# Kernel tuning notes

Measured on AMD Instinct MI355X. Metric: run time of the kernel, lower is better.

The kernel has to match this reference:

```python
import jax, jax.numpy as jnp
import numpy as np

B, S, D_IN, D_OUT = 4, 2048, 1024, 1024

def setup_inputs() -> dict:
    key = jax.random.key(0)
    k0, k1, k2, k3 = jax.random.split(key, 4)
    sc = 1.0 / np.sqrt(D_IN)
    return {
        "x": jax.random.normal(k0, (B, S, D_IN), dtype=jnp.float32),
        "wq": jax.random.normal(k1, (D_OUT, D_IN), dtype=jnp.float32) * sc,
        "wk": jax.random.normal(k2, (D_OUT, D_IN), dtype=jnp.float32) * sc,
        "wv": jax.random.normal(k3, (D_OUT, D_IN), dtype=jnp.float32) * sc,
    }

def reference(x, wq, wk, wv):
    # Linear (no bias): y = x @ W.T, W shaped [d_out, d_in]
    q = jnp.einsum("bsd,ed->bse", x, wq)
    k = jnp.einsum("bsd,ed->bse", x, wk)
    v = jnp.einsum("bsd,ed->bse", x, wv)
    scores = jnp.einsum("bqe,bke->bqk", q, k)  # [B,S,S]
    n = x.shape[1]
    causal = jnp.triu(jnp.ones((n, n), dtype=bool), k=1)  # True above diagonal -> masked
    scores = jnp.where(causal, -jnp.inf, scores)
    attn = jax.nn.softmax(scores / jnp.sqrt(jnp.asarray(k.shape[-1], scores.dtype)), axis=-1)
    # dropout p=0.0 -> identity
    return jnp.einsum("bqk,bke->bqe", attn, v)
```

## Files before the change

kernel.cpp:

```cpp
#include <hip/hip_runtime.h>

#define Bb 4
#define Ss 2048
#define Dd 1024

typedef unsigned short u16;
typedef __bf16 bf16x8 __attribute__((ext_vector_type(8)));
typedef float  f32x4  __attribute__((ext_vector_type(4)));

__device__ inline u16 f2bf(float f) {
  union { float f; unsigned u; } x; x.f = f;
  unsigned u = x.u;
  return (u16)((u + 0x7fffu + ((u >> 16) & 1u)) >> 16);
}
__device__ inline float bf2f(u16 h) {
  union { unsigned u; float f; } x; x.u = ((unsigned)h) << 16;
  return x.f;
}

__device__ static inline void gl_lds16(const u16* g, u16* l) {
  __builtin_amdgcn_global_load_lds((__attribute__((address_space(1))) const void*)g,
                                   (__attribute__((address_space(3))) void*)l,
                                   16, 0, 0);
}

__global__ __launch_bounds__(256) void cast_all(const float* __restrict__ x,
                                                const float* __restrict__ wq,
                                                const float* __restrict__ wk,
                                                const float* __restrict__ wv,
                                                u16* __restrict__ xb,
                                                u16* __restrict__ wb,
                                                float* __restrict__ lsum) {
  int id = blockIdx.x;
  if (id < 8) {
    float4 z = {0.f, 0.f, 0.f, 0.f};
    ((float4*)lsum)[id * 256 + threadIdx.x] = z;
  }
  const float* src; u16* dst; int off;
  if (id < 2048) {
    src = x; dst = xb; off = id * 4096;
  } else {
    int wi = id - 2048;
    int w = wi >> 8;
    src = (w == 0) ? wq : (w == 1) ? wk : wv;
    dst = wb + (size_t)w * Dd * Dd;
    off = (wi & 255) * 4096;
  }
#pragma unroll
  for (int t = 0; t < 4; t++) {
    int i = off + t * 1024 + threadIdx.x * 4;
    float4 v = *(const float4*)(src + i);
    unsigned p0 = (unsigned)f2bf(v.x) | ((unsigned)f2bf(v.y) << 16);
    unsigned p1 = (unsigned)f2bf(v.z) | ((unsigned)f2bf(v.w) << 16);
    uint2 p; p.x = p0; p.y = p1;
    *(uint2*)(dst + i) = p;
  }
}

#define BM 128
#define BN 128

__device__ inline void gemm_tile(const u16* __restrict__ A, int lda,
                                 const u16* __restrict__ Bp, int ldb,
                                 int kBeg, int kEnd,
                                 u16* lds, f32x4 acc[4][4]) {
  u16* lA0 = lds;
  u16* lB0 = lds + 4096;
  u16* lA1 = lds + 8192;
  u16* lB1 = lds + 12288;
  const int tid  = threadIdx.x;
  const int lane = tid & 63, wave = tid >> 6;
  const int quad = lane >> 4, r16 = lane & 15;
  const int wm = (wave & 1) * 64, wn = (wave >> 1) * 64;
  const int r0 = tid >> 2, part = tid & 3;

  for (int k0 = kBeg; k0 < kEnd; k0 += 64) {
    __syncthreads();
#pragma unroll
    for (int q = 0; q < 2; q++) {
      int row = q * 64 + r0;
      int s8 = (q * 256 + tid) * 8;
      const u16* ga = A  + (size_t)row * lda + k0 + part * 8;
      const u16* gb = Bp + (size_t)row * ldb + k0 + part * 8;
      gl_lds16(ga,      lA0 + s8);
      gl_lds16(gb,      lB0 + s8);
      gl_lds16(ga + 32, lA1 + s8);
      gl_lds16(gb + 32, lB1 + s8);
    }
    __syncthreads();
#pragma unroll
    for (int h = 0; h < 2; h++) {
      const u16* la = h ? lA1 : lA0;
      const u16* lb = h ? lB1 : lB0;
      bf16x8 fa[4], fb[4];
#pragma unroll
      for (int t = 0; t < 4; t++)
        fa[t] = *(const bf16x8*)(la + (wm + t * 16 + r16) * 32 + quad * 8);
#pragma unroll
      for (int t = 0; t < 4; t++)
        fb[t] = *(const bf16x8*)(lb + (wn + t * 16 + r16) * 32 + quad * 8);
#pragma unroll
      for (int tm = 0; tm < 4; tm++)
#pragma unroll
        for (int tn = 0; tn < 4; tn++)
          acc[tm][tn] = __builtin_amdgcn_mfma_f32_16x16x32_bf16(fa[tm], fb[tn],
                                                                acc[tm][tn], 0, 0, 0);
    }
  }
}

__global__ __launch_bounds__(256) void qkv_gemm(const u16* __restrict__ xb,
                                                const u16* __restrict__ wb,
                                                u16* __restrict__ qkv) {
  __shared__ __align__(16) u16 shmem[16384];
  const int id  = blockIdx.x;
  const int xcd = id & 7, j = id >> 3;
  const int xt  = j & 7;
  const int yl  = (j >> 3) & 7;
  const int zi  = j >> 6;
  const int y   = xcd * 8 + yl;
  const int row0 = y * BM;
  const int col0 = xt * BN;
  const u16* A  = xb + (size_t)row0 * Dd;
  const u16* Bp = wb + (size_t)zi * Dd * Dd + (size_t)col0 * Dd;
  f32x4 acc[4][4];
  const f32x4 zero = {0.f, 0.f, 0.f, 0.f};
#pragma unroll
  for (int tm = 0; tm < 4; tm++)
#pragma unroll
    for (int tn = 0; tn < 4; tn++) acc[tm][tn] = zero;

  gemm_tile(A, Dd, Bp, Dd, 0, Dd, shmem, acc);

  u16* out = qkv + (size_t)zi * ((size_t)Bb * Ss * Dd);
  const int lane = threadIdx.x & 63, wave = threadIdx.x >> 6;
  const int quad = lane >> 4, r16 = lane & 15;
  const int wm = (wave & 1) * 64, wn = (wave >> 1) * 64;
#pragma unroll
  for (int tm = 0; tm < 4; tm++)
#pragma unroll
    for (int tn = 0; tn < 4; tn++) {
      int rr = row0 + wm + tm * 16 + quad * 4;
      int cc = col0 + wn + tn * 16 + r16;
#pragma unroll
      for (int r = 0; r < 4; r++)
        out[(size_t)(rr + r) * Dd + cc] = f2bf(acc[tm][tn][r]);
    }
}

__global__ __launch_bounds__(256) void scores_fused(const u16* __restrict__ qb,
                                                    const u16* __restrict__ kb,
                                                    const u16* __restrict__ vb,
                                                    u16* __restrict__ sc,
                                                    u16* __restrict__ vt,
                                                    float* __restrict__ lsum) {
  __shared__ __align__(16) u16 shmem[16384];
  const int id = blockIdx.x;
  const int tid = threadIdx.x;

  if (id >= 544) {
    const int bid = id - 544;
    u16 (*t)[72] = (u16(*)[72])shmem;
    for (int u = bid; u < 2048; u += 480) {
      const int b = u >> 9, rem = u & 511;
      const int e0 = (rem >> 5) * 64, s0 = (rem & 31) * 64;
      const u16* src = vb + (size_t)b * Ss * Dd;
      u16* dst = vt + (size_t)b * Dd * Ss;
      if (u != bid) __syncthreads();
#pragma unroll
      for (int gg = tid; gg < 512; gg += 256) {
        int row = gg >> 3, prt = gg & 7;
        uint4 v = *(const uint4*)(src + (size_t)(s0 + row) * Dd + e0 + prt * 8);
        const u16* pv = (const u16*)&v;
#pragma unroll
        for (int jj = 0; jj < 8; jj++) t[prt * 8 + jj][row] = pv[jj];
      }
      __syncthreads();
#pragma unroll
      for (int gg = tid; gg < 512; gg += 256) {
        int ee = gg >> 3, prt = gg & 7;
        uint4 v = *(const uint4*)(&t[ee][prt * 8]);
        *(uint4*)(dst + (size_t)(e0 + ee) * Ss + s0 + prt * 8) = v;
      }
    }
    return;
  }

  const int xcd = id & 7, j = id >> 3;
  const int b = j / 17, tloc = j - b * 17;
  const int t = xcd * 17 + tloc;
  int it = (int)((sqrtf(8.f * (float)t + 1.f) - 1.f) * 0.5f);
  while ((it + 1) * (it + 2) / 2 <= t) it++;
  while (it * (it + 1) / 2 > t) it--;
  const int jt = t - it * (it + 1) / 2;

  const u16* A  = qb + (size_t)b * Ss * Dd + (size_t)it * BM * Dd;
  const u16* Bp = kb + (size_t)b * Ss * Dd + (size_t)jt * BN * Dd;
  f32x4 acc[4][4];
  const f32x4 zero = {0.f, 0.f, 0.f, 0.f};
#pragma unroll
  for (int tm = 0; tm < 4; tm++)
#pragma unroll
    for (int tn = 0; tn < 4; tn++) acc[tm][tn] = zero;

  gemm_tile(A, Dd, Bp, Dd, 0, Dd, shmem, acc);

  u16* out = sc + (size_t)b * Ss * Ss;
  float* lr = lsum + (size_t)b * Ss;
  const int lane = tid & 63, wave = tid >> 6;
  const int quad = lane >> 4, r16 = lane & 15;
  const int wm = (wave & 1) * 64, wn = (wave >> 1) * 64;
#pragma unroll
  for (int tm = 0; tm < 4; tm++) {
    float psum[4] = {0.f, 0.f, 0.f, 0.f};
#pragma unroll
    for (int tn = 0; tn < 4; tn++) {
      int rr = it * BM + wm + tm * 16 + quad * 4;
      int cc = jt * BN + wn + tn * 16 + r16;
#pragma unroll
      for (int r = 0; r < 4; r++) {
        float p = 0.f;
        u16 h = 0;
        if (cc <= rr + r) {
          h = f2bf(__expf(acc[tm][tn][r] * 0.03125f));
          p = bf2f(h);
        }
        out[(size_t)(rr + r) * Ss + cc] = h;
        psum[r] += p;
      }
    }
#pragma unroll
    for (int r = 0; r < 4; r++) {
      float s = psum[r];
      s += __shfl_xor(s, 1);
      s += __shfl_xor(s, 2);
      s += __shfl_xor(s, 4);
      s += __shfl_xor(s, 8);
      if (r16 == 0) {
        int row = it * BM + wm + tm * 16 + quad * 4 + r;
        atomicAdd(&lr[row], s);
      }
    }
  }
}

__global__ __launch_bounds__(256) void pv_gemm(const u16* __restrict__ sc,
                                               const u16* __restrict__ vt,
                                               const float* __restrict__ lsum,
                                               float* __restrict__ out) {
  __shared__ __align__(16) u16 shmem[16384];
  const int idx = blockIdx.x;
  const int xcd = idx & 7, slot = idx >> 3;
  const int qp = slot >> 3, col = slot & 7;
  const int b = qp & 3;
  const int it = (qp >> 2) ? (15 - xcd) : xcd;
  const int row0 = it * BM;
  const int col0 = col * BN;
  const u16* A  = sc + (size_t)b * Ss * Ss + (size_t)row0 * Ss;
  const u16* Bp = vt + (size_t)b * Dd * Ss + (size_t)col0 * Ss;
  f32x4 acc[4][4];
  const f32x4 zero = {0.f, 0.f, 0.f, 0.f};
#pragma unroll
  for (int tm = 0; tm < 4; tm++)
#pragma unroll
    for (int tn = 0; tn < 4; tn++) acc[tm][tn] = zero;

  gemm_tile(A, Ss, Bp, Ss, 0, row0 + BM, shmem, acc);

  float* o = out + (size_t)b * Ss * Dd;
  const float* lr = lsum + (size_t)b * Ss;
  const int lane = threadIdx.x & 63, wave = threadIdx.x >> 6;
  const int quad = lane >> 4, r16 = lane & 15;
  const int wm = (wave & 1) * 64, wn = (wave >> 1) * 64;
#pragma unroll
  for (int tm = 0; tm < 4; tm++) {
    int rbase = row0 + wm + tm * 16 + quad * 4;
    float s0 = 1.f / lr[rbase], s1 = 1.f / lr[rbase + 1];
    float s2 = 1.f / lr[rbase + 2], s3 = 1.f / lr[rbase + 3];
#pragma unroll
    for (int tn = 0; tn < 4; tn++) {
      int cc = col0 + wn + tn * 16 + r16;
      o[(size_t)(rbase + 0) * Dd + cc] = acc[tm][tn][0] * s0;
      o[(size_t)(rbase + 1) * Dd + cc] = acc[tm][tn][1] * s1;
      o[(size_t)(rbase + 2) * Dd + cc] = acc[tm][tn][2] * s2;
      o[(size_t)(rbase + 3) * Dd + cc] = acc[tm][tn][3] * s3;
    }
  }
}

extern "C" void kernel_launch(void* const* d_in, const int* in_sizes, int n_in,
                              void* d_out, int out_size, void* d_ws, size_t ws_size,
                              hipStream_t stream) {
  const float* x  = (const float*)d_in[0];
  const float* wq = (const float*)d_in[1];
  const float* wk = (const float*)d_in[2];
  const float* wv = (const float*)d_in[3];
  float* out = (float*)d_out;
  char* ws = (char*)d_ws;
  if (ws_size < 106987520u) return;

  u16* qkv  = (u16*)(ws);
  u16* sc   = (u16*)(ws + 50331648u);
  u16* xb   = (u16*)(ws + 83886080u);
  u16* vt   = xb;
  u16* wb   = (u16*)(ws + 100663296u);
  float* lsum = (float*)(ws + 106954752u);

  const size_t nQ = (size_t)Bb * Ss * Dd;

  cast_all<<<2816, 256, 0, stream>>>(x, wq, wk, wv, xb, wb, lsum);
  qkv_gemm<<<1536, 256, 0, stream>>>(xb, wb, qkv);
  scores_fused<<<1024, 256, 0, stream>>>(qkv, qkv + nQ, qkv + 2 * nQ, sc, vt, lsum);
  pv_gemm<<<512, 256, 0, stream>>>(sc, vt, lsum, out);
}
```

Before: 233.8 us.

## Replace QKV GEMM with 256x256-tile, 8-wave, 4-stage pipelined kernel

Replaces the 128x128-tile QKV projection GEMM with a 256x256-tile kernel of 512 threads. It uses a 4-deep LDS ring buffer fed by global_load_lds, an XOR-swizzled LDS layout and explicit vmcnt waits, so loads for later K steps overlap the MFMA work. Each half-tile of MFMAs is wrapped in s_setprio, and block ids are remapped so blocks are spread across XCDs. Larger tiles raise operand reuse and cut global traffic, but they use 128KB of LDS and more registers, which limits occupancy and leaves only 384 blocks.

```diff
diff --git a/kernel.cpp b/kernel.cpp
--- a/kernel.cpp
+++ b/kernel.cpp
@@ -22,6 +22,19 @@
   __builtin_amdgcn_global_load_lds((__attribute__((address_space(1))) const void*)g,
                                    (__attribute__((address_space(3))) void*)l,
                                    16, 0, 0);
+}
+
+__device__ static inline void qbar() {
+  asm volatile("" ::: "memory");
+  __builtin_amdgcn_s_barrier();
+  asm volatile("" ::: "memory");
+}
+
+template <int GATEN>
+__device__ __forceinline__ void qk_gate() {
+  if constexpr (GATEN == 8) asm volatile("s_waitcnt vmcnt(8)" ::: "memory");
+  else if constexpr (GATEN == 4) asm volatile("s_waitcnt vmcnt(4)" ::: "memory");
+  else if constexpr (GATEN == 0) asm volatile("s_waitcnt vmcnt(0)" ::: "memory");
 }
 
 __global__ __launch_bounds__(256) void cast_all(const float* __restrict__ x,
@@ -109,43 +122,114 @@
   }
 }
 
-__global__ __launch_bounds__(256) void qkv_gemm(const u16* __restrict__ xb,
-                                                const u16* __restrict__ wb,
-                                                u16* __restrict__ qkv) {
-  __shared__ __align__(16) u16 shmem[16384];
+#define QBK 32
+
+__global__ __launch_bounds__(512, 2) void qkv_gemm256(const u16* __restrict__ xb,
+                                                      const u16* __restrict__ wb,
+                                                      u16* __restrict__ qkv) {
+  __shared__ __align__(16) u16 sh[4 * 16384];
+  u16* const shf = sh;
+
   const int id  = blockIdx.x;
-  const int xcd = id & 7, j = id >> 3;
-  const int xt  = j & 7;
-  const int yl  = (j >> 3) & 7;
-  const int zi  = j >> 6;
-  const int y   = xcd * 8 + yl;
-  const int row0 = y * BM;
-  const int col0 = xt * BN;
+  const int swz = (id & 7) * 48 + (id >> 3);
+  const int zi  = swz >> 7;
+  const int rem = swz & 127;
+  const int mt  = rem >> 2, nt = rem & 3;
+  const int row0 = mt * 256, col0 = nt * 256;
   const u16* A  = xb + (size_t)row0 * Dd;
   const u16* Bp = wb + (size_t)zi * Dd * Dd + (size_t)col0 * Dd;
-  f32x4 acc[4][4];
-  const f32x4 zero = {0.f, 0.f, 0.f, 0.f};
-#pragma unroll
-  for (int tm = 0; tm < 4; tm++)
-#pragma unroll
-    for (int tn = 0; tn < 4; tn++) acc[tm][tn] = zero;
-
-  gemm_tile(A, Dd, Bp, Dd, 0, Dd, shmem, acc);
+
+  const int tid  = threadIdx.x;
+  const int lane = tid & 63, wave = tid >> 6;
+  const int wr = wave >> 2, wc = wave & 3;
+  const int quad = lane >> 4, r16 = lane & 15;
+
+  const int pA0 = tid, pA1 = tid + 512;
+  const int r0a = pA0 >> 2, c0a = pA0 & 3;
+  const int r1a = pA1 >> 2, c1a = pA1 & 3;
+  const u16* aS0 = A  + (size_t)r0a * Dd + (size_t)((c0a ^ ((r0a >> 1) & 3)) * 8);
+  const u16* aS1 = A  + (size_t)r1a * Dd + (size_t)((c1a ^ ((r1a >> 1) & 3)) * 8);
+  const u16* bS0 = Bp + (size_t)r0a * Dd + (size_t)((c0a ^ ((r0a >> 1) & 3)) * 8);
+  const u16* bS1 = Bp + (size_t)r1a * Dd + (size_t)((c1a ^ ((r1a >> 1) & 3)) * 8);
+
+  auto stgA = [&](int S) {
+    u16* d = shf + (S & 3) * 16384;
+    gl_lds16(aS0 + (size_t)S * QBK, d + pA0 * 8);
+    gl_lds16(aS1 + (size_t)S * QBK, d + pA1 * 8);
+  };
+  auto stgB = [&](int S) {
+    u16* d = shf + (S & 3) * 16384 + 8192;
+    gl_lds16(bS0 + (size_t)S * QBK, d + pA0 * 8);
+    gl_lds16(bS1 + (size_t)S * QBK, d + pA1 * 8);
+  };
+
+  const int chq  = (quad ^ ((r16 >> 1) & 3)) * 8;
+  const int idxA = (wr * 128 + r16) * 32 + chq;
+  const int idxB = (wc * 64  + r16) * 32 + chq;
+
+  f32x4 acc[8][4];
+#pragma unroll
+  for (int m = 0; m < 8; m++)
+#pragma unroll
+    for (int n = 0; n < 4; n++) acc[m][n] = (f32x4){0.f, 0.f, 0.f, 0.f};
+  bf16x8 fb[4];
+
+#define QKV_TILE(U, STG_S, GATEN)                                              \
+  {                                                                            \
+    const u16* lA = shf + (U) * 16384;                                         \
+    const u16* lB = lA + 8192;                                                 \
+    bf16x8 fa[4];                                                              \
+    _Pragma("unroll") for (int m = 0; m < 4; m++)                              \
+        fa[m] = *(const bf16x8*)(lA + idxA + m * 512);                         \
+    _Pragma("unroll") for (int n = 0; n < 4; n++)                              \
+        fb[n] = *(const bf16x8*)(lB + idxB + n * 512);                         \
+    if ((STG_S) >= 0) stgA(STG_S);                                             \
+    qbar();                                                                    \
+    __builtin_amdgcn_s_setprio(1);                                             \
+    _Pragma("unroll") for (int m = 0; m < 4; m++)                              \
+      _Pragma("unroll") for (int n = 0; n < 4; n++)                            \
+        acc[m][n] = __builtin_amdgcn_mfma_f32_16x16x32_bf16(fa[m], fb[n],      \
+                                                            acc[m][n], 0, 0, 0); \
+    __builtin_amdgcn_s_setprio(0);                                             \
+    qbar();                                                                    \
+    _Pragma("unroll") for (int m = 0; m < 4; m++)                              \
+        fa[m] = *(const bf16x8*)(lA + idxA + (m + 4) * 512);                   \
+    if ((STG_S) >= 0) stgB(STG_S);                                             \
+    qk_gate<GATEN>();                                                          \
+    qbar();                                                                    \
+    __builtin_amdgcn_s_setprio(1);                                             \
+    _Pragma("unroll") for (int m = 0; m < 4; m++)                              \
+      _Pragma("unroll") for (int n = 0; n < 4; n++)                            \
+        acc[m + 4][n] = __builtin_amdgcn_mfma_f32_16x16x32_bf16(fa[m], fb[n],  \
+                                                                acc[m + 4][n], 0, 0, 0); \
+    __builtin_amdgcn_s_setprio(0);                                             \
+    qbar();                                                                    \
+  }
+
+  stgA(0); stgB(0); stgA(1); stgB(1); stgA(2); stgB(2);
+  asm volatile("s_waitcnt vmcnt(8)" ::: "memory");
+  qbar();
+
+#pragma unroll 1
+  for (int T = 0; T < 28; T++) QKV_TILE(T & 3, T + 3, 8);
+  QKV_TILE(0, 31, 8);
+  QKV_TILE(1, -1, 4);
+  QKV_TILE(2, -1, 0);
+  QKV_TILE(3, -1, -1);
+#undef QKV_TILE
 
   u16* out = qkv + (size_t)zi * ((size_t)Bb * Ss * Dd);
-  const int lane = threadIdx.x & 63, wave = threadIdx.x >> 6;
-  const int quad = lane >> 4, r16 = lane & 15;
-  const int wm = (wave & 1) * 64, wn = (wave >> 1) * 64;
-#pragma unroll
-  for (int tm = 0; tm < 4; tm++)
-#pragma unroll
-    for (int tn = 0; tn < 4; tn++) {
-      int rr = row0 + wm + tm * 16 + quad * 4;
-      int cc = col0 + wn + tn * 16 + r16;
+#pragma unroll
+  for (int m = 0; m < 8; m++) {
+    int rr = row0 + wr * 128 + m * 16 + quad * 4;
+#pragma unroll
+    for (int n = 0; n < 4; n++) {
+      int cc = col0 + wc * 64 + n * 16 + r16;
 #pragma unroll
       for (int r = 0; r < 4; r++)
-        out[(size_t)(rr + r) * Dd + cc] = f2bf(acc[tm][tn][r]);
-    }
+        out[(size_t)(rr + r) * Dd + cc] = f2bf(acc[m][n][r]);
+    }
+  }
 }
 
 __global__ __launch_bounds__(256) void scores_fused(const u16* __restrict__ qb,
@@ -309,7 +393,7 @@
   const size_t nQ = (size_t)Bb * Ss * Dd;
 
   cast_all<<<2816, 256, 0, stream>>>(x, wq, wk, wv, xb, wb, lsum);
-  qkv_gemm<<<1536, 256, 0, stream>>>(xb, wb, qkv);
+  qkv_gemm256<<<384, 512, 0, stream>>>(xb, wb, qkv);
   scores_fused<<<1024, 256, 0, stream>>>(qkv, qkv + nQ, qkv + 2 * nQ, sc, vt, lsum);
   pv_gemm<<<512, 256, 0, stream>>>(sc, vt, lsum, out);
 }
```

New measurement: 242.6 us. 1.04x slower.
